# Performance work log

Measured on AMD Instinct MI355X. Metric: run time of the kernel, lower is better.

Reference implementation:

```python
import jax, jax.numpy as jnp
import numpy as np

B, S, D = 2, 2048, 2048
H, DH = 16, 128  # heads, dhead


def setup_inputs() -> dict:
    key = jax.random.key(0)
    k1, k2, k3 = jax.random.split(key, 3)
    x = jax.random.normal(k1, (B, S, D), dtype=jnp.float32)
    # torch Linear weights: [out_features, in_features], fan_in-scaled init
    w_in = jax.random.normal(k2, (3 * H * DH, D), dtype=jnp.float32) * (1.0 / np.sqrt(D))
    w_out = jax.random.normal(k3, (D, H * DH), dtype=jnp.float32) * (1.0 / np.sqrt(H * DH))
    return {"x": x, "w_in": w_in, "w_out": w_out}


def reference(x, w_in, w_out):
    b, s, _ = x.shape
    # input projection (no bias): [b, s, 3*H*DH]
    projected = jnp.einsum("bsd,ed->bse", x, w_in)
    # view(b, s, H, 3*DH) then chunk along last dim -> q, k, v each [b, s, H, DH]
    projected = projected.reshape(b, s, H, 3 * DH)
    q, k, v = jnp.split(projected, 3, axis=-1)
    # naive path: scores [b, H, s, s]
    scores = jnp.einsum("bqhd,bkhd->bhqk", q, k) * (1.0 / np.sqrt(DH))
    # causal mask (tril keeps, upper triangle -> -inf)
    causal_mask = jnp.tril(jnp.ones((s, s), dtype=bool))
    scores = jnp.where(causal_mask, scores, jnp.float32(-jnp.inf))
    attn = jax.nn.softmax(scores, axis=-1)
    # PV: [b, s, H, DH]
    out = jnp.einsum("bhqk,bkhd->bqhd", attn, v)
    out = out.reshape(b, s, H * DH)
    # output projection (no bias): [b, s, D]
    return jnp.einsum("bse,de->bsd", out, w_out)
```

## Files before the change

### kernel.cpp

```cpp
#include <hip/hip_runtime.h>
#include <hip/hip_bf16.h>
#include <math.h>


typedef short bf16x8 __attribute__((ext_vector_type(8)));
typedef float f32x4 __attribute__((ext_vector_type(4)));

#define NEG_BIG -30000.0f

__device__ __forceinline__ short f2bf(float f) {
    union { float f; unsigned u; } v; v.f = f;
    unsigned r = v.u + 0x7fffu + ((v.u >> 16) & 1u);
    return (short)(r >> 16);
}

__device__ __forceinline__ int pack2bf(float a, float b) {
    return (int)((((unsigned)f2bf(b)) << 16) | (((unsigned)f2bf(a)) & 0xffffu));
}

#define GLDS16(g, l) \
    __builtin_amdgcn_global_load_lds((const __attribute__((address_space(1))) void*)(g), \
                                     (__attribute__((address_space(3))) void*)(l), 16, 0, 0)

__global__ __launch_bounds__(256) void cvt_f32_bf16(const float* __restrict__ src,
                                                    short* __restrict__ dst, int n) {
    int i = (blockIdx.x * blockDim.x + threadIdx.x) * 4;
    if (i < n) {
        float4 v = *(const float4*)(src + i);
        short4 o;
        o.x = f2bf(v.x); o.y = f2bf(v.y); o.z = f2bf(v.z); o.w = f2bf(v.w);
        *(short4*)(dst + i) = o;
    }
}

template <int BN, bool F32OUT>
__global__ __launch_bounds__(256) void gemm_bt(const short* __restrict__ A,
                                               const short* __restrict__ Bm,
                                               void* __restrict__ Cv,
                                               int N, int K) {
    constexpr int NT = BN / 32;
    constexpr int SUBA = 128 * 32;
    constexpr int SUBB = BN * 32;
    __shared__ short sA[2 * SUBA];
    __shared__ short sB[2 * SUBB];
    const int lane = threadIdx.x & 63;
    const int w = threadIdx.x >> 6;
    const int l15 = lane & 15, quad = lane >> 4;
    const int bm0 = blockIdx.y * 128, bn0 = blockIdx.x * BN;

    const int c1 = w * 64 + lane;
    const short* gA = A + (size_t)(bm0 + (c1 >> 2)) * K + (c1 & 3) * 8;
    const short* gB = Bm + (size_t)(bn0 + (c1 >> 2)) * K + (c1 & 3) * 8;
    const size_t half64 = (size_t)64 * K;
    short* lA1 = sA + w * 512;
    short* lA2 = sA + 2048 + w * 512;
    short* lB1 = sB + w * 512;
    short* lB2 = sB + 2048 + w * 512;

    const int wm = (w >> 1) * 64, wn = (w & 1) * (BN / 2);
    const short* pa = sA + (wm + l15) * 32 + quad * 8;
    const short* pb = sB + (wn + l15) * 32 + quad * 8;

    f32x4 acc[4][NT] = {};
    for (int k0 = 0; k0 < K; k0 += 64) {
        #pragma unroll
        for (int s = 0; s < 2; s++) {
            const int ks = k0 + s * 32;
            GLDS16(gA + ks, lA1 + s * SUBA);
            GLDS16(gA + half64 + ks, lA2 + s * SUBA);
            GLDS16(gB + ks, lB1 + s * SUBB);
            if constexpr (BN == 128) GLDS16(gB + half64 + ks, lB2 + s * SUBB);
        }
        __syncthreads();
        #pragma unroll
        for (int s = 0; s < 2; s++) {
            bf16x8 af[4], bf[NT];
            #pragma unroll
            for (int mt = 0; mt < 4; mt++) af[mt] = *(const bf16x8*)(pa + s * SUBA + mt * 512);
            #pragma unroll
            for (int nt = 0; nt < NT; nt++) bf[nt] = *(const bf16x8*)(pb + s * SUBB + nt * 512);
            #pragma unroll
            for (int mt = 0; mt < 4; mt++)
                #pragma unroll
                for (int nt = 0; nt < NT; nt++)
                    acc[mt][nt] = __builtin_amdgcn_mfma_f32_16x16x32_bf16(af[mt], bf[nt], acc[mt][nt], 0, 0, 0);
        }
        __syncthreads();
    }
    #pragma unroll
    for (int mt = 0; mt < 4; mt++)
        #pragma unroll
        for (int nt = 0; nt < NT; nt++)
            #pragma unroll
            for (int r = 0; r < 4; r++) {
                int row = bm0 + wm + mt * 16 + quad * 4 + r;
                int col = bn0 + wn + nt * 16 + l15;
                if (F32OUT)
                    ((float*)Cv)[(size_t)row * N + col] = acc[mt][nt][r];
                else
                    ((short*)Cv)[(size_t)row * N + col] = f2bf(acc[mt][nt][r]);
            }
}

#define VP2 72
__global__ __launch_bounds__(512) void attn_kernel(const short* __restrict__ P,
                                                   short* __restrict__ O) {
    constexpr int S = 2048, ROWW = 6144, HD = 2048;
    const int id = blockIdx.x;
    const int b = id >> 8;
    const int rr = id & 255;
    const int h = rr & 15;
    const int t0 = rr >> 4;
    const int qt = b ? (15 - t0) : t0;
    const int wave = threadIdx.x >> 6, lane = threadIdx.x & 63;
    const int l15 = lane & 15, quad = lane >> 4;
    const int qRow = qt * 128 + wave * 16;
    const short* Pb = P + (size_t)b * S * ROWW;
    const short* Qp = Pb + h * 384;
    const short* Kp = Qp + 128;
    const short* Vp = Qp + 256;

    __shared__ short sK[2][64 * 128];
    __shared__ short sVt[2][128 * VP2];

    bf16x8 qf[4];
    #pragma unroll
    for (int f = 0; f < 4; f++)
        qf[f] = *(const bf16x8*)(Qp + (size_t)(qRow + l15) * ROWW + f * 32 + quad * 8);

    const bool isK = wave < 4;
    const int c1 = (wave & 3) * 64 + lane;
    const int krow1 = c1 >> 4;
    const int kcol = ((c1 & 15) ^ (krow1 & 15)) * 8;
    const short* gK1 = Kp + (size_t)krow1 * ROWW + kcol;
    const short* gK2 = Kp + (size_t)(krow1 + 16) * ROWW + kcol;
    const short* gK3 = Kp + (size_t)(krow1 + 32) * ROWW + kcol;
    const short* gK4 = Kp + (size_t)(krow1 + 48) * ROWW + kcol;
    const int ldsOff1 = (wave & 3) * 512;
    const int ldsOff2 = 2048 + ldsOff1;
    const int ldsOff3 = 4096 + ldsOff1;
    const int ldsOff4 = 6144 + ldsOff1;
    const int vt = (int)threadIdx.x - 256;
    const int vKey = vt & 31;
    const int vD0 = (vt >> 5) * 8;
    const short* gV = Vp + (size_t)vKey * ROWW + vD0;
    const short* gV2 = Vp + (size_t)(vKey + 32) * ROWW + vD0;

    const int kTiles = qt * 2 + 2;
    const float scale = 0.08838834764831845f;
    const int qG = qRow + l15;

    f32x4 accO[8] = {};
    float m_i = NEG_BIG, l_i = 0.f;

    if (isK) {
        GLDS16(gK1, &sK[0][ldsOff1]);
        GLDS16(gK2, &sK[0][ldsOff2]);
        GLDS16(gK3, &sK[0][ldsOff3]);
        GLDS16(gK4, &sK[0][ldsOff4]);
    } else {
        bf16x8 v0 = *(const bf16x8*)(gV);
        bf16x8 v1 = *(const bf16x8*)(gV + 64);
        bf16x8 v2 = *(const bf16x8*)(gV2);
        bf16x8 v3 = *(const bf16x8*)(gV2 + 64);
        #pragma unroll
        for (int j = 0; j < 8; j++) {
            sVt[0][(vD0 + j) * VP2 + vKey] = v0[j];
            sVt[0][(vD0 + 64 + j) * VP2 + vKey] = v1[j];
            sVt[0][(vD0 + j) * VP2 + vKey + 32] = v2[j];
            sVt[0][(vD0 + 64 + j) * VP2 + vKey + 32] = v3[j];
        }
    }
    __syncthreads();

    for (int kt = 0; kt < kTiles; kt++) {
        const int cur = kt & 1, nxt = cur ^ 1;
        const bool pre = (kt + 1 < kTiles);
        bf16x8 v0n, v1n, v2n, v3n;
        if (pre) {
            const size_t kOff = (size_t)(kt + 1) * 64 * ROWW;
            if (isK) {
                GLDS16(gK1 + kOff, &sK[nxt][ldsOff1]);
                GLDS16(gK2 + kOff, &sK[nxt][ldsOff2]);
                GLDS16(gK3 + kOff, &sK[nxt][ldsOff3]);
                GLDS16(gK4 + kOff, &sK[nxt][ldsOff4]);
            } else {
                v0n = *(const bf16x8*)(gV + kOff);
                v1n = *(const bf16x8*)(gV + kOff + 64);
                v2n = *(const bf16x8*)(gV2 + kOff);
                v3n = *(const bf16x8*)(gV2 + kOff + 64);
            }
        }
        if (kt * 64 <= qRow + 15) {
            f32x4 sc[4] = {};
            #pragma unroll
            for (int f = 0; f < 4; f++) {
                const int jj = ((4 * f + quad) ^ l15) * 8;
                #pragma unroll
                for (int hh = 0; hh < 4; hh++) {
                    bf16x8 kf = *(const bf16x8*)(&sK[cur][(hh * 16 + l15) * 128 + jj]);
                    sc[hh] = __builtin_amdgcn_mfma_f32_16x16x32_bf16(kf, qf[f], sc[hh], 0, 0, 0);
                }
            }
            #pragma unroll
            for (int hh = 0; hh < 4; hh++)
                #pragma unroll
                for (int r = 0; r < 4; r++) {
                    int key = kt * 64 + hh * 16 + quad * 4 + r;
                    float v = sc[hh][r] * scale;
                    sc[hh][r] = (key <= qG) ? v : NEG_BIG;
                }
            float mloc = sc[0][0];
            #pragma unroll
            for (int hh = 0; hh < 4; hh++)
                #pragma unroll
                for (int r = 0; r < 4; r++) mloc = fmaxf(mloc, sc[hh][r]);
            mloc = fmaxf(mloc, __shfl_xor(mloc, 16));
            mloc = fmaxf(mloc, __shfl_xor(mloc, 32));
            if (!__all(mloc <= m_i + 8.0f)) {
                const float nm = fmaxf(m_i, mloc);
                const float alpha = __expf(m_i - nm);
                m_i = nm;
                l_i *= alpha;
                #pragma unroll
                for (int t = 0; t < 8; t++)
                    #pragma unroll
                    for (int r = 0; r < 4; r++) accO[t][r] *= alpha;
            }
            float ssum = 0.f;
            #pragma unroll
            for (int hh = 0; hh < 4; hh++)
                #pragma unroll
                for (int r = 0; r < 4; r++) {
                    float p = __expf(sc[hh][r] - m_i);
                    sc[hh][r] = p;
                    ssum += p;
                }
            ssum += __shfl_xor(ssum, 16);
            ssum += __shfl_xor(ssum, 32);
            l_i += ssum;
            #pragma unroll
            for (int s = 0; s < 2; s++) {
                const int d00 = pack2bf(sc[2 * s][0], sc[2 * s][1]);
                const int d01 = pack2bf(sc[2 * s][2], sc[2 * s][3]);
                const int d10 = pack2bf(sc[2 * s + 1][0], sc[2 * s + 1][1]);
                const int d11 = pack2bf(sc[2 * s + 1][2], sc[2 * s + 1][3]);
                const int srcA = l15 + ((quad & 1) << 5);
                const int srcB = srcA + 16;
                const int s00 = __shfl(d00, srcA), s01 = __shfl(d01, srcA);
                const int s02 = __shfl(d00, srcB), s03 = __shfl(d01, srcB);
                const int s10 = __shfl(d10, srcA), s11 = __shfl(d11, srcA);
                const int s12 = __shfl(d10, srcB), s13 = __shfl(d11, srcB);
                union { int i[4]; bf16x8 v; } pu;
                const bool lo = quad < 2;
                pu.i[0] = lo ? s00 : s10;
                pu.i[1] = lo ? s01 : s11;
                pu.i[2] = lo ? s02 : s12;
                pu.i[3] = lo ? s03 : s13;
                const bf16x8 pf = pu.v;
                #pragma unroll
                for (int t = 0; t < 8; t++) {
                    bf16x8 vf = *(const bf16x8*)(&sVt[cur][(t * 16 + l15) * VP2 + s * 32 + quad * 8]);
                    accO[t] = __builtin_amdgcn_mfma_f32_16x16x32_bf16(vf, pf, accO[t], 0, 0, 0);
                }
            }
        }
        if (pre && !isK) {
            #pragma unroll
            for (int j = 0; j < 8; j++) {
                sVt[nxt][(vD0 + j) * VP2 + vKey] = v0n[j];
                sVt[nxt][(vD0 + 64 + j) * VP2 + vKey] = v1n[j];
                sVt[nxt][(vD0 + j) * VP2 + vKey + 32] = v2n[j];
                sVt[nxt][(vD0 + 64 + j) * VP2 + vKey + 32] = v3n[j];
            }
        }
        __syncthreads();
    }
    const float inv = 1.0f / l_i;
    #pragma unroll
    for (int t = 0; t < 8; t++) {
        short4 st;
        st.x = f2bf(accO[t][0] * inv);
        st.y = f2bf(accO[t][1] * inv);
        st.z = f2bf(accO[t][2] * inv);
        st.w = f2bf(accO[t][3] * inv);
        *(short4*)(&O[(size_t)(b * S + qG) * HD + h * 128 + t * 16 + quad * 4]) = st;
    }
}

extern "C" void kernel_launch(void* const* d_in, const int* in_sizes, int n_in,
                              void* d_out, int out_size, void* d_ws, size_t ws_size,
                              hipStream_t stream) {
    const float* x     = (const float*)d_in[0];
    const float* w_in  = (const float*)d_in[1];
    const float* w_out = (const float*)d_in[2];
    float* out = (float*)d_out;

    short* Pbuf   = (short*)d_ws;
    short* xObuf  = Pbuf  + (size_t)4096 * 6144;
    short* winb   = xObuf + (size_t)8388608;
    short* woutb  = winb  + (size_t)6144 * 2048;

    dim3 blk(256, 1, 1);
    const int nx = 2 * 2048 * 2048, nwi = 6144 * 2048, nwo = 2048 * 2048;
    hipLaunchKernelGGL(cvt_f32_bf16, dim3(nx / 1024), blk, 0, stream, x, xObuf, nx);
    hipLaunchKernelGGL(cvt_f32_bf16, dim3(nwi / 1024), blk, 0, stream, w_in, winb, nwi);
    hipLaunchKernelGGL(cvt_f32_bf16, dim3(nwo / 1024), blk, 0, stream, w_out, woutb, nwo);
    hipLaunchKernelGGL((gemm_bt<128, false>), dim3(48, 16, 1), blk, 0, stream,
                       xObuf, winb, (void*)Pbuf, 6144, 2048);
    hipLaunchKernelGGL((gemm_bt<128, false>), dim3(48, 16, 1), blk, 0, stream,
                       xObuf + (size_t)2048 * 2048, winb,
                       (void*)(Pbuf + (size_t)2048 * 6144), 6144, 2048);
    hipLaunchKernelGGL(attn_kernel, dim3(512, 1, 1), dim3(512, 1, 1), 0, stream, Pbuf, xObuf);
    hipLaunchKernelGGL((gemm_bt<128, true>), dim3(16, 32, 1), blk, 0, stream, xObuf, woutb, (void*)out, 2048, 2048);
}
```

Baseline: 388.5 us.

## Process two 16-row query tiles per wave in attention, halving block size

The attention kernel now runs 4 waves of 256 threads, and each wave handles 32 query rows as two independent 16-row MFMA tiles. This lets each K/V fragment read from LDS feed two MFMAs and halves the number of waves loading shared tiles. It also skips the causal mask on fully visible tiles, folds the scale into the exponent, and writes V into the transposed LDS buffer with vectorised short4 stores. The cost is higher register pressure from doubled accumulators, which may reduce occupancy.

```diff
diff --git a/kernel.cpp b/kernel.cpp
--- a/kernel.cpp
+++ b/kernel.cpp
@@ -103,7 +103,7 @@
 }
 
 #define VP2 72
-__global__ __launch_bounds__(512) void attn_kernel(const short* __restrict__ P,
+__global__ __launch_bounds__(256) void attn_kernel(const short* __restrict__ P,
                                                    short* __restrict__ O) {
     constexpr int S = 2048, ROWW = 6144, HD = 2048;
     const int id = blockIdx.x;
@@ -114,7 +114,7 @@
     const int qt = b ? (15 - t0) : t0;
     const int wave = threadIdx.x >> 6, lane = threadIdx.x & 63;
     const int l15 = lane & 15, quad = lane >> 4;
-    const int qRow = qt * 128 + wave * 16;
+    const int qRow = qt * 128 + wave * 32;
     const short* Pb = P + (size_t)b * S * ROWW;
     const short* Qp = Pb + h * 384;
     const short* Kp = Qp + 128;
@@ -123,52 +123,52 @@
     __shared__ short sK[2][64 * 128];
     __shared__ short sVt[2][128 * VP2];
 
-    bf16x8 qf[4];
+    bf16x8 qf0[4], qf1[4];
     #pragma unroll
-    for (int f = 0; f < 4; f++)
-        qf[f] = *(const bf16x8*)(Qp + (size_t)(qRow + l15) * ROWW + f * 32 + quad * 8);
-
-    const bool isK = wave < 4;
-    const int c1 = (wave & 3) * 64 + lane;
-    const int krow1 = c1 >> 4;
-    const int kcol = ((c1 & 15) ^ (krow1 & 15)) * 8;
-    const short* gK1 = Kp + (size_t)krow1 * ROWW + kcol;
-    const short* gK2 = Kp + (size_t)(krow1 + 16) * ROWW + kcol;
-    const short* gK3 = Kp + (size_t)(krow1 + 32) * ROWW + kcol;
-    const short* gK4 = Kp + (size_t)(krow1 + 48) * ROWW + kcol;
-    const int ldsOff1 = (wave & 3) * 512;
-    const int ldsOff2 = 2048 + ldsOff1;
-    const int ldsOff3 = 4096 + ldsOff1;
-    const int ldsOff4 = 6144 + ldsOff1;
-    const int vt = (int)threadIdx.x - 256;
-    const int vKey = vt & 31;
-    const int vD0 = (vt >> 5) * 8;
-    const short* gV = Vp + (size_t)vKey * ROWW + vD0;
-    const short* gV2 = Vp + (size_t)(vKey + 32) * ROWW + vD0;
+    for (int f = 0; f < 4; f++) {
+        qf0[f] = *(const bf16x8*)(Qp + (size_t)(qRow + l15) * ROWW + f * 32 + quad * 8);
+        qf1[f] = *(const bf16x8*)(Qp + (size_t)(qRow + 16 + l15) * ROWW + f * 32 + quad * 8);
+    }
+
+    const bool isK = wave < 2;
+    const int c1 = (wave & 1) * 64 + lane;
+    const int krow = c1 >> 4;
+    const int chunk = c1 & 15;
+    const short* gKe = Kp + (size_t)krow * ROWW + (chunk ^ krow) * 8;
+    const short* gKo = Kp + (size_t)(krow + 8) * ROWW + (chunk ^ (krow + 8)) * 8;
+    const int kBase = (wave & 1) * 512;
+    const int vt = (int)threadIdx.x - 128;
+    const int vk0 = (vt & 15) * 4;
+    const int vd0 = (vt >> 4) * 16;
+    const short* gV0 = Vp + (size_t)vk0 * ROWW + vd0;
 
     const int kTiles = qt * 2 + 2;
     const float scale = 0.08838834764831845f;
-    const int qG = qRow + l15;
-
-    f32x4 accO[8] = {};
-    float m_i = NEG_BIG, l_i = 0.f;
-
+    const float THRR = 90.50966799f;
+    const int qG0 = qRow + l15, qG1 = qRow + 16 + l15;
+
+    f32x4 accO0[8] = {}, accO1[8] = {};
+    float m0 = NEG_BIG, l0 = 0.f, m1 = NEG_BIG, l1 = 0.f;
+
+    bf16x8 vA[4], vB[4];
     if (isK) {
-        GLDS16(gK1, &sK[0][ldsOff1]);
-        GLDS16(gK2, &sK[0][ldsOff2]);
-        GLDS16(gK3, &sK[0][ldsOff3]);
-        GLDS16(gK4, &sK[0][ldsOff4]);
+        #pragma unroll
+        for (int s2 = 0; s2 < 4; s2++) {
+            GLDS16(gKe + (size_t)(16 * s2) * ROWW, &sK[0][s2 * 2048 + kBase]);
+            GLDS16(gKo + (size_t)(16 * s2) * ROWW, &sK[0][s2 * 2048 + 1024 + kBase]);
+        }
     } else {
-        bf16x8 v0 = *(const bf16x8*)(gV);
-        bf16x8 v1 = *(const bf16x8*)(gV + 64);
-        bf16x8 v2 = *(const bf16x8*)(gV2);
-        bf16x8 v3 = *(const bf16x8*)(gV2 + 64);
+        #pragma unroll
+        for (int i = 0; i < 4; i++) {
+            vA[i] = *(const bf16x8*)(gV0 + (size_t)i * ROWW);
+            vB[i] = *(const bf16x8*)(gV0 + (size_t)i * ROWW + 8);
+        }
         #pragma unroll
         for (int j = 0; j < 8; j++) {
-            sVt[0][(vD0 + j) * VP2 + vKey] = v0[j];
-            sVt[0][(vD0 + 64 + j) * VP2 + vKey] = v1[j];
-            sVt[0][(vD0 + j) * VP2 + vKey + 32] = v2[j];
-            sVt[0][(vD0 + 64 + j) * VP2 + vKey + 32] = v3[j];
+            short4 w0; w0.x = vA[0][j]; w0.y = vA[1][j]; w0.z = vA[2][j]; w0.w = vA[3][j];
+            *(short4*)(&sVt[0][(vd0 + j) * VP2 + vk0]) = w0;
+            short4 w1; w1.x = vB[0][j]; w1.y = vB[1][j]; w1.z = vB[2][j]; w1.w = vB[3][j];
+            *(short4*)(&sVt[0][(vd0 + 8 + j) * VP2 + vk0]) = w1;
         }
     }
     __syncthreads();
@@ -176,115 +176,172 @@
     for (int kt = 0; kt < kTiles; kt++) {
         const int cur = kt & 1, nxt = cur ^ 1;
         const bool pre = (kt + 1 < kTiles);
-        bf16x8 v0n, v1n, v2n, v3n;
         if (pre) {
             const size_t kOff = (size_t)(kt + 1) * 64 * ROWW;
             if (isK) {
-                GLDS16(gK1 + kOff, &sK[nxt][ldsOff1]);
-                GLDS16(gK2 + kOff, &sK[nxt][ldsOff2]);
-                GLDS16(gK3 + kOff, &sK[nxt][ldsOff3]);
-                GLDS16(gK4 + kOff, &sK[nxt][ldsOff4]);
+                #pragma unroll
+                for (int s2 = 0; s2 < 4; s2++) {
+                    GLDS16(gKe + kOff + (size_t)(16 * s2) * ROWW, &sK[nxt][s2 * 2048 + kBase]);
+                    GLDS16(gKo + kOff + (size_t)(16 * s2) * ROWW, &sK[nxt][s2 * 2048 + 1024 + kBase]);
+                }
             } else {
-                v0n = *(const bf16x8*)(gV + kOff);
-                v1n = *(const bf16x8*)(gV + kOff + 64);
-                v2n = *(const bf16x8*)(gV2 + kOff);
-                v3n = *(const bf16x8*)(gV2 + kOff + 64);
-            }
-        }
-        if (kt * 64 <= qRow + 15) {
-            f32x4 sc[4] = {};
+                #pragma unroll
+                for (int i = 0; i < 4; i++) {
+                    vA[i] = *(const bf16x8*)(gV0 + kOff + (size_t)i * ROWW);
+                    vB[i] = *(const bf16x8*)(gV0 + kOff + (size_t)i * ROWW + 8);
+                }
+            }
+        }
+        if (kt * 64 <= qRow + 31) {
+            f32x4 s0[4] = {}, s1[4] = {};
             #pragma unroll
             for (int f = 0; f < 4; f++) {
                 const int jj = ((4 * f + quad) ^ l15) * 8;
                 #pragma unroll
                 for (int hh = 0; hh < 4; hh++) {
                     bf16x8 kf = *(const bf16x8*)(&sK[cur][(hh * 16 + l15) * 128 + jj]);
-                    sc[hh] = __builtin_amdgcn_mfma_f32_16x16x32_bf16(kf, qf[f], sc[hh], 0, 0, 0);
-                }
-            }
-            #pragma unroll
-            for (int hh = 0; hh < 4; hh++)
-                #pragma unroll
-                for (int r = 0; r < 4; r++) {
-                    int key = kt * 64 + hh * 16 + quad * 4 + r;
-                    float v = sc[hh][r] * scale;
-                    sc[hh][r] = (key <= qG) ? v : NEG_BIG;
-                }
-            float mloc = sc[0][0];
-            #pragma unroll
-            for (int hh = 0; hh < 4; hh++)
-                #pragma unroll
-                for (int r = 0; r < 4; r++) mloc = fmaxf(mloc, sc[hh][r]);
-            mloc = fmaxf(mloc, __shfl_xor(mloc, 16));
-            mloc = fmaxf(mloc, __shfl_xor(mloc, 32));
-            if (!__all(mloc <= m_i + 8.0f)) {
-                const float nm = fmaxf(m_i, mloc);
-                const float alpha = __expf(m_i - nm);
-                m_i = nm;
-                l_i *= alpha;
-                #pragma unroll
-                for (int t = 0; t < 8; t++)
-                    #pragma unroll
-                    for (int r = 0; r < 4; r++) accO[t][r] *= alpha;
-            }
-            float ssum = 0.f;
-            #pragma unroll
-            for (int hh = 0; hh < 4; hh++)
-                #pragma unroll
-                for (int r = 0; r < 4; r++) {
-                    float p = __expf(sc[hh][r] - m_i);
-                    sc[hh][r] = p;
-                    ssum += p;
-                }
-            ssum += __shfl_xor(ssum, 16);
-            ssum += __shfl_xor(ssum, 32);
-            l_i += ssum;
-            #pragma unroll
-            for (int s = 0; s < 2; s++) {
-                const int d00 = pack2bf(sc[2 * s][0], sc[2 * s][1]);
-                const int d01 = pack2bf(sc[2 * s][2], sc[2 * s][3]);
-                const int d10 = pack2bf(sc[2 * s + 1][0], sc[2 * s + 1][1]);
-                const int d11 = pack2bf(sc[2 * s + 1][2], sc[2 * s + 1][3]);
+                    s0[hh] = __builtin_amdgcn_mfma_f32_16x16x32_bf16(kf, qf0[f], s0[hh], 0, 0, 0);
+                    s1[hh] = __builtin_amdgcn_mfma_f32_16x16x32_bf16(kf, qf1[f], s1[hh], 0, 0, 0);
+                }
+            }
+            if (!(kt * 64 + 63 <= qRow)) {
+                #pragma unroll
+                for (int hh = 0; hh < 4; hh++)
+                    #pragma unroll
+                    for (int r = 0; r < 4; r++) {
+                        const int key = kt * 64 + hh * 16 + quad * 4 + r;
+                        if (key > qG0) s0[hh][r] = NEG_BIG;
+                        if (key > qG1) s1[hh][r] = NEG_BIG;
+                    }
+            }
+            {
+                float ml = s0[0][0];
+                #pragma unroll
+                for (int hh = 0; hh < 4; hh++)
+                    #pragma unroll
+                    for (int r = 0; r < 4; r++) ml = fmaxf(ml, s0[hh][r]);
+                ml = fmaxf(ml, __shfl_xor(ml, 16));
+                ml = fmaxf(ml, __shfl_xor(ml, 32));
+                if (!__all(ml <= m0 + THRR)) {
+                    const float nm = fmaxf(m0, ml);
+                    const float al = __expf((m0 - nm) * scale);
+                    m0 = nm; l0 *= al;
+                    #pragma unroll
+                    for (int t = 0; t < 8; t++)
+                        #pragma unroll
+                        for (int r = 0; r < 4; r++) accO0[t][r] *= al;
+                }
+                float ss = 0.f;
+                #pragma unroll
+                for (int hh = 0; hh < 4; hh++)
+                    #pragma unroll
+                    for (int r = 0; r < 4; r++) {
+                        float p = __expf((s0[hh][r] - m0) * scale);
+                        s0[hh][r] = p; ss += p;
+                    }
+                ss += __shfl_xor(ss, 16);
+                ss += __shfl_xor(ss, 32);
+                l0 += ss;
+            }
+            {
+                float ml = s1[0][0];
+                #pragma unroll
+                for (int hh = 0; hh < 4; hh++)
+                    #pragma unroll
+                    for (int r = 0; r < 4; r++) ml = fmaxf(ml, s1[hh][r]);
+                ml = fmaxf(ml, __shfl_xor(ml, 16));
+                ml = fmaxf(ml, __shfl_xor(ml, 32));
+                if (!__all(ml <= m1 + THRR)) {
+                    const float nm = fmaxf(m1, ml);
+                    const float al = __expf((m1 - nm) * scale);
+                    m1 = nm; l1 *= al;
+                    #pragma unroll
+                    for (int t = 0; t < 8; t++)
+                        #pragma unroll
+                        for (int r = 0; r < 4; r++) accO1[t][r] *= al;
+                }
+                float ss = 0.f;
+                #pragma unroll
+                for (int hh = 0; hh < 4; hh++)
+                    #pragma unroll
+                    for (int r = 0; r < 4; r++) {
+                        float p = __expf((s1[hh][r] - m1) * scale);
+                        s1[hh][r] = p; ss += p;
+                    }
+                ss += __shfl_xor(ss, 16);
+                ss += __shfl_xor(ss, 32);
+                l1 += ss;
+            }
+            #pragma unroll
+            for (int sl = 0; sl < 2; sl++) {
                 const int srcA = l15 + ((quad & 1) << 5);
                 const int srcB = srcA + 16;
-                const int s00 = __shfl(d00, srcA), s01 = __shfl(d01, srcA);
-                const int s02 = __shfl(d00, srcB), s03 = __shfl(d01, srcB);
-                const int s10 = __shfl(d10, srcA), s11 = __shfl(d11, srcA);
-                const int s12 = __shfl(d10, srcB), s13 = __shfl(d11, srcB);
-                union { int i[4]; bf16x8 v; } pu;
                 const bool lo = quad < 2;
-                pu.i[0] = lo ? s00 : s10;
-                pu.i[1] = lo ? s01 : s11;
-                pu.i[2] = lo ? s02 : s12;
-                pu.i[3] = lo ? s03 : s13;
-                const bf16x8 pf = pu.v;
+                const int a00 = pack2bf(s0[2 * sl][0], s0[2 * sl][1]);
+                const int a01 = pack2bf(s0[2 * sl][2], s0[2 * sl][3]);
+                const int a10 = pack2bf(s0[2 * sl + 1][0], s0[2 * sl + 1][1]);
+                const int a11 = pack2bf(s0[2 * sl + 1][2], s0[2 * sl + 1][3]);
+                union { int i[4]; bf16x8 v; } p0;
+                {
+                    const int t00 = __shfl(a00, srcA), t01 = __shfl(a01, srcA);
+                    const int t02 = __shfl(a00, srcB), t03 = __shfl(a01, srcB);
+                    const int t10 = __shfl(a10, srcA), t11 = __shfl(a11, srcA);
+                    const int t12 = __shfl(a10, srcB), t13 = __shfl(a11, srcB);
+                    p0.i[0] = lo ? t00 : t10;
+                    p0.i[1] = lo ? t01 : t11;
+                    p0.i[2] = lo ? t02 : t12;
+                    p0.i[3] = lo ? t03 : t13;
+                }
+                const int b00 = pack2bf(s1[2 * sl][0], s1[2 * sl][1]);
+                const int b01 = pack2bf(s1[2 * sl][2], s1[2 * sl][3]);
+                const int b10 = pack2bf(s1[2 * sl + 1][0], s1[2 * sl + 1][1]);
+                const int b11 = pack2bf(s1[2 * sl + 1][2], s1[2 * sl + 1][3]);
+                union { int i[4]; bf16x8 v; } p1;
+                {
+                    const int t00 = __shfl(b00, srcA), t01 = __shfl(b01, srcA);
+                    const int t02 = __shfl(b00, srcB), t03 = __shfl(b01, srcB);
+                    const int t10 = __shfl(b10, srcA), t11 = __shfl(b11, srcA);
+                    const int t12 = __shfl(b10, srcB), t13 = __shfl(b11, srcB);
+                    p1.i[0] = lo ? t00 : t10;
+                    p1.i[1] = lo ? t01 : t11;
+                    p1.i[2] = lo ? t02 : t12;
+                    p1.i[3] = lo ? t03 : t13;
+                }
                 #pragma unroll
                 for (int t = 0; t < 8; t++) {
-                    bf16x8 vf = *(const bf16x8*)(&sVt[cur][(t * 16 + l15) * VP2 + s * 32 + quad * 8]);
-                    accO[t] = __builtin_amdgcn_mfma_f32_16x16x32_bf16(vf, pf, accO[t], 0, 0, 0);
+                    bf16x8 vf = *(const bf16x8*)(&sVt[cur][(t * 16 + l15) * VP2 + sl * 32 + quad * 8]);
+                    accO0[t] = __builtin_amdgcn_mfma_f32_16x16x32_bf16(vf, p0.v, accO0[t], 0, 0, 0);
+                    accO1[t] = __builtin_amdgcn_mfma_f32_16x16x32_bf16(vf, p1.v, accO1[t], 0, 0, 0);
                 }
             }
         }
         if (pre && !isK) {
             #pragma unroll
             for (int j = 0; j < 8; j++) {
-                sVt[nxt][(vD0 + j) * VP2 + vKey] = v0n[j];
-                sVt[nxt][(vD0 + 64 + j) * VP2 + vKey] = v1n[j];
-                sVt[nxt][(vD0 + j) * VP2 + vKey + 32] = v2n[j];
-                sVt[nxt][(vD0 + 64 + j) * VP2 + vKey + 32] = v3n[j];
+                short4 w0; w0.x = vA[0][j]; w0.y = vA[1][j]; w0.z = vA[2][j]; w0.w = vA[3][j];
+                *(short4*)(&sVt[nxt][(vd0 + j) * VP2 + vk0]) = w0;
+                short4 w1; w1.x = vB[0][j]; w1.y = vB[1][j]; w1.z = vB[2][j]; w1.w = vB[3][j];
+                *(short4*)(&sVt[nxt][(vd0 + 8 + j) * VP2 + vk0]) = w1;
             }
         }
         __syncthreads();
     }
-    const float inv = 1.0f / l_i;
+    const float inv0 = 1.0f / l0;
+    const float inv1 = 1.0f / l1;
     #pragma unroll
     for (int t = 0; t < 8; t++) {
         short4 st;
-        st.x = f2bf(accO[t][0] * inv);
-        st.y = f2bf(accO[t][1] * inv);
-        st.z = f2bf(accO[t][2] * inv);
-        st.w = f2bf(accO[t][3] * inv);
-        *(short4*)(&O[(size_t)(b * S + qG) * HD + h * 128 + t * 16 + quad * 4]) = st;
+        st.x = f2bf(accO0[t][0] * inv0);
+        st.y = f2bf(accO0[t][1] * inv0);
+        st.z = f2bf(accO0[t][2] * inv0);
+        st.w = f2bf(accO0[t][3] * inv0);
+        *(short4*)(&O[(size_t)(b * S + qG0) * HD + h * 128 + t * 16 + quad * 4]) = st;
+        short4 su;
+        su.x = f2bf(accO1[t][0] * inv1);
+        su.y = f2bf(accO1[t][1] * inv1);
+        su.z = f2bf(accO1[t][2] * inv1);
+        su.w = f2bf(accO1[t][3] * inv1);
+        *(short4*)(&O[(size_t)(b * S + qG1) * HD + h * 128 + t * 16 + quad * 4]) = su;
     }
 }
 
@@ -311,6 +368,6 @@
     hipLaunchKernelGGL((gemm_bt<128, false>), dim3(48, 16, 1), blk, 0, stream,
                        xObuf + (size_t)2048 * 2048, winb,
                        (void*)(Pbuf + (size_t)2048 * 6144), 6144, 2048);
-    hipLaunchKernelGGL(attn_kernel, dim3(512, 1, 1), dim3(512, 1, 1), 0, stream, Pbuf, xObuf);
+    hipLaunchKernelGGL(attn_kernel, dim3(512, 1, 1), dim3(256, 1, 1), 0, stream, Pbuf, xObuf);
     hipLaunchKernelGGL((gemm_bt<128, true>), dim3(16, 32, 1), blk, 0, stream, xObuf, woutb, (void*)out, 2048, 2048);
 }
```

Result: slower. 404.1 us (+4.0%).
